# Performance work log

Measured on AMD Instinct MI355X. Metric: run time of the kernel, lower is better.

The kernel has to match this reference:

```python
import jax, jax.numpy as jnp
import numpy as np

ASIZE, VSIZE, HSIZE, MSIZE = 128, 512, 512, 48


def _xavier(key, shape):
    fan_in, fan_out = shape[1], shape[0]
    limit = float(np.sqrt(6.0 / (fan_in + fan_out)))
    return jax.random.uniform(key, shape, jnp.float32, -limit, limit)


def setup_inputs() -> dict:
    key = jax.random.key(0)
    ks = jax.random.split(key, 9)
    B, T = 32, 64
    audio = jax.random.normal(ks[0], (B, T, ASIZE), jnp.float32)
    video = jax.random.normal(ks[1], (B, T, MSIZE, VSIZE), jnp.float32)
    return {
        "audio": audio,
        "video": video,
        "W_audio": _xavier(ks[2], (HSIZE, ASIZE)),
        "b_audio": jnp.zeros((HSIZE,), jnp.float32),
        "W_video": _xavier(ks[3], (HSIZE, VSIZE)),
        "b_video": jnp.zeros((HSIZE,), jnp.float32),
        "W_v": _xavier(ks[4], (MSIZE, HSIZE)),
        "W_g": _xavier(ks[5], (MSIZE, HSIZE)),
        "W_h": _xavier(ks[6], (1, MSIZE)),
    }


def reference(audio, video, W_audio, b_audio, W_video, b_video, W_v, W_g, W_h):
    B, T, N, vsize = video.shape  # N == MSIZE == 48 required by the broadcast
    V = video.reshape(B * T, N, vsize)                      # [BT, N, vsize]
    v = jax.nn.relu(jnp.einsum('bnv,hv->bnh', V, W_video) + b_video)  # [BT,N,h]
    a = jax.nn.relu(audio.reshape(-1, audio.shape[-1]) @ W_audio.T + b_audio)  # [BT,h]
    inter = a @ W_g.T                                        # [BT, m]
    # torch broadcast: [BT,N,m] + [BT,m,1] with N==m -> inter indexed by spatial pos
    content = jnp.einsum('bnh,mh->bnm', v, W_v) + inter[:, :, None]
    z = jnp.einsum('bnm,om->bno', jnp.tanh(content), W_h)[..., 0]  # [BT, N]
    alpha = jax.nn.softmax(z, axis=-1)                        # [BT, N]
    c = jnp.einsum('bn,bnv->bv', alpha, V)                    # [BT, vsize]
    return c.reshape(B, T, vsize)
```

## Files before the change

kernel.cpp:

```cpp
#include <hip/hip_runtime.h>
#include <hip/hip_bf16.h>

typedef __bf16 bf16x8 __attribute__((ext_vector_type(8)));
typedef __bf16 bf16x4 __attribute__((ext_vector_type(4)));
typedef float  f32x4  __attribute__((ext_vector_type(4)));

#define BT    2048
#define MDIM  48

#define WS_WVID  0
#define WS_WV    (512*512*2)
#define WS_WG    (WS_WV + 48*512*2)
#define WS_INTER (WS_WG + 48*512*2)

__global__ __launch_bounds__(256) void convert_weights(
    const float* __restrict__ Wvid, const float* __restrict__ Wv,
    const float* __restrict__ Wg,
    __bf16* __restrict__ wvid_k, __bf16* __restrict__ wv_b,
    __bf16* __restrict__ wg_b) {
    int i = blockIdx.x * blockDim.x + threadIdx.x;
    const int nv = 65536, n2 = 6144;
    if (i < nv) {
        int h = i >> 7, k4 = i & 127;
        float4 f = ((const float4*)Wvid)[i];
        bf16x4 o = {(__bf16)f.x, (__bf16)f.y, (__bf16)f.z, (__bf16)f.w};
        *(bf16x4*)(wvid_k + (size_t)(((k4 >> 1) * 512 + h) * 8 + (k4 & 1) * 4)) = o;
    } else if (i < nv + n2) {
        int j = i - nv;
        float4 f = ((const float4*)Wv)[j];
        bf16x4 o = {(__bf16)f.x, (__bf16)f.y, (__bf16)f.z, (__bf16)f.w};
        ((bf16x4*)wv_b)[j] = o;
    } else {
        int j = i - nv - n2;
        float4 f = ((const float4*)Wg)[j];
        bf16x4 o = {(__bf16)f.x, (__bf16)f.y, (__bf16)f.z, (__bf16)f.w};
        ((bf16x4*)wg_b)[j] = o;
    }
}

__global__ __launch_bounds__(512) void audio_batch(
    const float* __restrict__ audio, const float* __restrict__ Wa,
    const float* __restrict__ ba, const __bf16* __restrict__ wg_b,
    float* __restrict__ inter) {
    __shared__ float  ain[16 * 128];
    __shared__ __bf16 as_s[64 * 17 * 8];

    const int bt0 = blockIdx.x * 16;
    const int t   = threadIdx.x;

    ((float4*)ain)[t] = ((const float4*)(audio + (size_t)bt0 * 128))[t];
    __syncthreads();

    float acc[16];
    float bias = ba[t];
    #pragma unroll
    for (int b = 0; b < 16; ++b) acc[b] = bias;
    const float4* wr = (const float4*)(Wa + (size_t)t * 128);
    #pragma unroll 4
    for (int k4 = 0; k4 < 32; ++k4) {
        float4 wv = wr[k4];
        #pragma unroll
        for (int b = 0; b < 16; ++b) {
            float4 av = ((const float4*)ain)[b * 32 + k4];
            acc[b] += av.x*wv.x + av.y*wv.y + av.z*wv.z + av.w*wv.w;
        }
    }
    #pragma unroll
    for (int b = 0; b < 16; ++b)
        as_s[(((t >> 3) * 17 + b) << 3) | (t & 7)] = (__bf16)fmaxf(acc[b], 0.f);
    __syncthreads();

    const int w = t >> 6, lane = t & 63, l16 = lane & 15, quad = lane >> 4;
    if (w < 3) {
        f32x4 c = {0.f, 0.f, 0.f, 0.f};
        const __bf16* bp = wg_b + (size_t)(w * 16 + l16) * 512 + quad * 8;
        const __bf16* ap = &as_s[((quad * 17 + l16)) * 8];
        bf16x8 aC = *(const bf16x8*)ap;
        bf16x8 bC = *(const bf16x8*)bp;
        #pragma unroll
        for (int kt = 0; kt < 16; ++kt) {
            bf16x8 aN, bN;
            if (kt < 15) {
                aN = *(const bf16x8*)(ap + (kt + 1) * (4 * 17 * 8));
                bN = *(const bf16x8*)(bp + (kt + 1) * 32);
            }
            c = __builtin_amdgcn_mfma_f32_16x16x32_bf16(aC, bC, c, 0, 0, 0);
            if (kt < 15) { aC = aN; bC = bN; }
        }
        #pragma unroll
        for (int r = 0; r < 4; ++r)
            inter[(size_t)(bt0 + quad * 4 + r) * 48 + w * 16 + l16] = c[r];
    }
}

__global__ __launch_bounds__(512, 4) void main_fused(
    const float* __restrict__ video, const float* __restrict__ bvid,
    const __bf16* __restrict__ wvid_k, const __bf16* __restrict__ wv_b,
    const float* __restrict__ Wh, const float* __restrict__ inter_g,
    float* __restrict__ out) {

    __shared__ uint4 pool4[3136];
    __shared__ float inter_s[MDIM];
    __shared__ float z_s[MDIM];
    __shared__ float alpha_s[MDIM];
    __shared__ float content8[256];

    char* pool = (char*)pool4;

    const int bt   = blockIdx.x;
    const int tid  = threadIdx.x;
    const int w    = tid >> 6;
    const int lane = tid & 63;
    const int l16  = lane & 15;
    const int quad = lane >> 4;

    const float* Vg = video + (size_t)bt * (48 * 512);
    const char*  bbase = (const char*)wvid_k;

    if (tid < MDIM) { inter_s[tid] = inter_g[bt * MDIM + tid]; z_s[tid] = 0.f; }
    if (tid < 256) content8[tid] = 0.f;

    #pragma unroll
    for (int p = 0; p < 6; ++p) {
        int g  = tid + p * 512;
        int s  = g >> 6;
        int kc = g & 63;
        const float4* s4 = (const float4*)(Vg + s * 512 + kc * 8);
        float4 x = s4[0], y = s4[1];
        bf16x8 gr = {(__bf16)x.x, (__bf16)x.y, (__bf16)x.z, (__bf16)x.w,
                     (__bf16)y.x, (__bf16)y.y, (__bf16)y.z, (__bf16)y.w};
        *(bf16x8*)(pool + (kc * 49 + s) * 16) = gr;
    }
    __syncthreads();

    f32x4 acc[3][4];
    #pragma unroll
    for (int mt = 0; mt < 3; ++mt)
        #pragma unroll
        for (int j = 0; j < 4; ++j) {
            f32x4 z = {0.f, 0.f, 0.f, 0.f};
            acc[mt][j] = z;
        }
    {
        const int bIdx0 = quad * 8192 + (w * 64 + l16) * 16;
        bf16x8 bC[4];
        #pragma unroll
        for (int j = 0; j < 4; ++j)
            bC[j] = *(const bf16x8*)(bbase + bIdx0 + j * 256);

        #pragma unroll
        for (int kt = 0; kt < 16; ++kt) {
            bf16x8 bN[4];
            if (kt < 15) {
                #pragma unroll
                for (int j = 0; j < 4; ++j)
                    bN[j] = *(const bf16x8*)(bbase + bIdx0 + (kt + 1) * 32768 + j * 256);
            }
            bf16x8 a[3];
            #pragma unroll
            for (int mt = 0; mt < 3; ++mt)
                a[mt] = *(const bf16x8*)(pool + ((4 * kt + quad) * 49 + mt * 16 + l16) * 16);
            #pragma unroll
            for (int mt = 0; mt < 3; ++mt)
                #pragma unroll
                for (int j = 0; j < 4; ++j)
                    acc[mt][j] = __builtin_amdgcn_mfma_f32_16x16x32_bf16(
                                     a[mt], bC[j], acc[mt][j], 0, 0, 0);
            if (kt < 15) {
                #pragma unroll
                for (int j = 0; j < 4; ++j) bC[j] = bN[j];
            }
        }
    }
    __syncthreads();

    #pragma unroll
    for (int j = 0; j < 4; ++j) {
        int h = w * 64 + j * 16 + l16;
        float bias = bvid[h];
        #pragma unroll
        for (int mt = 0; mt < 3; ++mt) {
            #pragma unroll
            for (int r = 0; r < 4; ++r) {
                int s = mt * 16 + quad * 4 + r;
                *(__bf16*)(pool + s * 1040 + h * 2) =
                    (__bf16)fmaxf(acc[mt][j][r] + bias, 0.f);
            }
        }
    }
    __syncthreads();

    {
        int ti = w / 3, tj = w - ti * 3;
        const __bf16* bp = wv_b + (size_t)(tj * 16 + l16) * 512 + quad * 8;
        const char*   ap = pool + (ti * 16 + l16) * 1040 + quad * 16;
        f32x4 c3 = {0.f, 0.f, 0.f, 0.f};
        bf16x8 aC = *(const bf16x8*)ap;
        bf16x8 bC = *(const bf16x8*)bp;
        #pragma unroll
        for (int kt = 0; kt < 16; ++kt) {
            bf16x8 aN, bN;
            if (kt < 15) {
                aN = *(const bf16x8*)(ap + (kt + 1) * 64);
                bN = *(const bf16x8*)(bp + (kt + 1) * 32);
            }
            c3 = __builtin_amdgcn_mfma_f32_16x16x32_bf16(aC, bC, c3, 0, 0, 0);
            if (kt < 15) { aC = aN; bC = bN; }
        }
        float wh = Wh[tj * 16 + l16];
        #pragma unroll
        for (int r = 0; r < 4; ++r) {
            int s = ti * 16 + quad * 4 + r;
            float contrib = tanhf(c3[r] + inter_s[s]) * wh;
            contrib += __shfl_xor(contrib, 1);
            contrib += __shfl_xor(contrib, 2);
            contrib += __shfl_xor(contrib, 4);
            contrib += __shfl_xor(contrib, 8);
            if (l16 == 0) atomicAdd(&z_s[s], contrib);
        }
        f32x4 p8 = {0.f, 0.f, 0.f, 0.f};
        #pragma unroll
        for (int q = 0; q < 2; ++q) {
            int kt = 2 * w + q;
            bf16x8 a8 = *(const bf16x8*)(pool + (32 + l16) * 1040 + kt * 64 + quad * 16);
            bf16x8 b8 = *(const bf16x8*)(wv_b + (size_t)(32 + l16) * 512 + kt * 32 + quad * 8);
            p8 = __builtin_amdgcn_mfma_f32_16x16x32_bf16(a8, b8, p8, 0, 0, 0);
        }
        #pragma unroll
        for (int r = 0; r < 4; ++r)
            atomicAdd(&content8[(quad * 4 + r) * 16 + l16], p8[r]);
    }
    __syncthreads();

    if (w == 0) {
        float wh = Wh[32 + l16];
        #pragma unroll
        for (int r = 0; r < 4; ++r) {
            int s = 32 + quad * 4 + r;
            float contrib = tanhf(content8[(quad * 4 + r) * 16 + l16] + inter_s[s]) * wh;
            contrib += __shfl_xor(contrib, 1);
            contrib += __shfl_xor(contrib, 2);
            contrib += __shfl_xor(contrib, 4);
            contrib += __shfl_xor(contrib, 8);
            if (l16 == 0) atomicAdd(&z_s[s], contrib);
        }
    }
    __syncthreads();

    if (w == 0) {
        float x = (lane < MDIM) ? z_s[lane] : -INFINITY;
        float mx = x;
        #pragma unroll
        for (int off = 32; off >= 1; off >>= 1) mx = fmaxf(mx, __shfl_xor(mx, off));
        float e = (lane < MDIM) ? expf(x - mx) : 0.f;
        float sm = e;
        #pragma unroll
        for (int off = 32; off >= 1; off >>= 1) sm += __shfl_xor(sm, off);
        if (lane < MDIM) alpha_s[lane] = e / sm;
    }
    __syncthreads();

    float acc5 = 0.f;
    #pragma unroll
    for (int s = 0; s < MDIM; ++s)
        acc5 += alpha_s[s] * Vg[s * 512 + tid];
    out[(size_t)bt * 512 + tid] = acc5;
}

extern "C" void kernel_launch(void* const* d_in, const int* in_sizes, int n_in,
                              void* d_out, int out_size, void* d_ws, size_t ws_size,
                              hipStream_t stream) {
    const float* audio   = (const float*)d_in[0];
    const float* video   = (const float*)d_in[1];
    const float* W_audio = (const float*)d_in[2];
    const float* b_audio = (const float*)d_in[3];
    const float* W_video = (const float*)d_in[4];
    const float* b_video = (const float*)d_in[5];
    const float* W_v     = (const float*)d_in[6];
    const float* W_g     = (const float*)d_in[7];
    const float* W_h     = (const float*)d_in[8];
    float* out = (float*)d_out;

    char* ws = (char*)d_ws;
    __bf16* wvid_k = (__bf16*)(ws + WS_WVID);
    __bf16* wv_b   = (__bf16*)(ws + WS_WV);
    __bf16* wg_b   = (__bf16*)(ws + WS_WG);
    float*  inter  = (float*)(ws + WS_INTER);

    convert_weights<<<304, 256, 0, stream>>>(W_video, W_v, W_g, wvid_k, wv_b, wg_b);
    audio_batch<<<BT / 16, 512, 0, stream>>>(audio, W_audio, b_audio, wg_b, inter);
    main_fused<<<BT, 512, 0, stream>>>(video, b_video, wvid_k, wv_b, W_h, inter, out);
}
```

Measured before the change: 400.1 us.

## Pipeline video tile staging with MFMA loop and split content accumulator chain

Stops staging the whole 48x512 video slab into shared memory before the first GEMM. The slab is now streamed in eight K-chunks, and the global loads for the next chunk are issued while the MFMAs on the current chunk run. The second small GEMM uses two independent accumulators so consecutive MFMAs do not wait on each other, and the occupancy hint in launch_bounds goes from 4 to 6. The trade-off is eight barriers per block instead of one, and the higher occupancy target may force register spills given the 48-register accumulator array.

```diff
diff --git a/kernel.cpp b/kernel.cpp
--- a/kernel.cpp
+++ b/kernel.cpp
@@ -93,7 +93,7 @@
     }
 }
 
-__global__ __launch_bounds__(512, 4) void main_fused(
+__global__ __launch_bounds__(512, 6) void main_fused(
     const float* __restrict__ video, const float* __restrict__ bvid,
     const __bf16* __restrict__ wvid_k, const __bf16* __restrict__ wv_b,
     const float* __restrict__ Wh, const float* __restrict__ inter_g,
@@ -120,18 +120,23 @@
     if (tid < MDIM) { inter_s[tid] = inter_g[bt * MDIM + tid]; z_s[tid] = 0.f; }
     if (tid < 256) content8[tid] = 0.f;
 
-    #pragma unroll
-    for (int p = 0; p < 6; ++p) {
-        int g  = tid + p * 512;
-        int s  = g >> 6;
-        int kc = g & 63;
-        const float4* s4 = (const float4*)(Vg + s * 512 + kc * 8);
-        float4 x = s4[0], y = s4[1];
-        bf16x8 gr = {(__bf16)x.x, (__bf16)x.y, (__bf16)x.z, (__bf16)x.w,
-                     (__bf16)y.x, (__bf16)y.y, (__bf16)y.z, (__bf16)y.w};
-        *(bf16x8*)(pool + (kc * 49 + s) * 16) = gr;
-    }
-    __syncthreads();
+    const int  s_a    = tid >> 3;
+    const int  kcl    = tid & 7;
+    const bool stager = (tid < 384);
+
+    if (stager) {
+        const float4* p4 = (const float4*)(Vg + s_a * 512 + kcl * 8);
+        float4 x = p4[0], y = p4[1];
+        bf16x8 g = {(__bf16)x.x, (__bf16)x.y, (__bf16)x.z, (__bf16)x.w,
+                    (__bf16)y.x, (__bf16)y.y, (__bf16)y.z, (__bf16)y.w};
+        *(bf16x8*)(pool + (kcl * 49 + s_a) * 16) = g;
+    }
+
+    const int bIdx0 = quad * 8192 + (w * 64 + l16) * 16;
+    bf16x8 bC[4];
+    #pragma unroll
+    for (int j = 0; j < 4; ++j)
+        bC[j] = *(const bf16x8*)(bbase + bIdx0 + j * 256);
 
     f32x4 acc[3][4];
     #pragma unroll
@@ -141,15 +146,19 @@
             f32x4 z = {0.f, 0.f, 0.f, 0.f};
             acc[mt][j] = z;
         }
-    {
-        const int bIdx0 = quad * 8192 + (w * 64 + l16) * 16;
-        bf16x8 bC[4];
-        #pragma unroll
-        for (int j = 0; j < 4; ++j)
-            bC[j] = *(const bf16x8*)(bbase + bIdx0 + j * 256);
-
-        #pragma unroll
-        for (int kt = 0; kt < 16; ++kt) {
+
+    __syncthreads();
+
+    #pragma unroll
+    for (int c = 0; c < 8; ++c) {
+        float4 sx, sy;
+        if (c < 7 && stager) {
+            const float4* p4 = (const float4*)(Vg + s_a * 512 + ((c + 1) * 8 + kcl) * 8);
+            sx = p4[0]; sy = p4[1];
+        }
+        #pragma unroll
+        for (int k = 0; k < 2; ++k) {
+            const int kt = c * 2 + k;
             bf16x8 bN[4];
             if (kt < 15) {
                 #pragma unroll
@@ -171,8 +180,13 @@
                 for (int j = 0; j < 4; ++j) bC[j] = bN[j];
             }
         }
-    }
-    __syncthreads();
+        if (c < 7 && stager) {
+            bf16x8 g = {(__bf16)sx.x, (__bf16)sx.y, (__bf16)sx.z, (__bf16)sx.w,
+                        (__bf16)sy.x, (__bf16)sy.y, (__bf16)sy.z, (__bf16)sy.w};
+            *(bf16x8*)(pool + (((c + 1) * 8 + kcl) * 49 + s_a) * 16) = g;
+        }
+        __syncthreads();
+    }
 
     #pragma unroll
     for (int j = 0; j < 4; ++j) {
@@ -194,19 +208,18 @@
         int ti = w / 3, tj = w - ti * 3;
         const __bf16* bp = wv_b + (size_t)(tj * 16 + l16) * 512 + quad * 8;
         const char*   ap = pool + (ti * 16 + l16) * 1040 + quad * 16;
-        f32x4 c3 = {0.f, 0.f, 0.f, 0.f};
-        bf16x8 aC = *(const bf16x8*)ap;
-        bf16x8 bC = *(const bf16x8*)bp;
-        #pragma unroll
-        for (int kt = 0; kt < 16; ++kt) {
-            bf16x8 aN, bN;
-            if (kt < 15) {
-                aN = *(const bf16x8*)(ap + (kt + 1) * 64);
-                bN = *(const bf16x8*)(bp + (kt + 1) * 32);
-            }
-            c3 = __builtin_amdgcn_mfma_f32_16x16x32_bf16(aC, bC, c3, 0, 0, 0);
-            if (kt < 15) { aC = aN; bC = bN; }
-        }
+        f32x4 c3e = {0.f, 0.f, 0.f, 0.f};
+        f32x4 c3o = {0.f, 0.f, 0.f, 0.f};
+        #pragma unroll
+        for (int kt = 0; kt < 16; kt += 2) {
+            bf16x8 a0 = *(const bf16x8*)(ap + kt * 64);
+            bf16x8 b0 = *(const bf16x8*)(bp + kt * 32);
+            c3e = __builtin_amdgcn_mfma_f32_16x16x32_bf16(a0, b0, c3e, 0, 0, 0);
+            bf16x8 a1 = *(const bf16x8*)(ap + (kt + 1) * 64);
+            bf16x8 b1 = *(const bf16x8*)(bp + (kt + 1) * 32);
+            c3o = __builtin_amdgcn_mfma_f32_16x16x32_bf16(a1, b1, c3o, 0, 0, 0);
+        }
+        f32x4 c3 = c3e + c3o;
         float wh = Wh[tj * 16 + l16];
         #pragma unroll
         for (int r = 0; r < 4; ++r) {
```

New measurement: 500.1 us. +25.0%, slower.
